# Kernel tuning notes

Measured on AMD Instinct MI355X. Metric: run time of the kernel, lower is better.

## Reference

```python
import jax, jax.numpy as jnp
import numpy as np

EPS = 1e-5


def conv1d(x, w, b):
    # x: (B, C_in, S), w: (C_out, C_in, K), 'same' padding = K//2
    pad = w.shape[-1] // 2
    y = jax.lax.conv_general_dilated(
        x, w, window_strides=(1,), padding=[(pad, pad)],
        dimension_numbers=("NCH", "OIH", "NCH"))
    return y + b[None, :, None]


def layer_norm(x, g, b):
    m = jnp.mean(x, axis=-1, keepdims=True)
    v = jnp.var(x, axis=-1, keepdims=True)
    return (x - m) * jax.lax.rsqrt(v + EPS) * g + b


def duration_predict(x, conv1_w, conv1_b, conv2_w, conv2_b,
                     ln1_g, ln1_b, ln2_g, ln2_b, lin_w, lin_b):
    # x: (B, S, C)
    out = conv1d(jnp.swapaxes(x, -2, -1), conv1_w, conv1_b)          # (B, F, S)
    out = jax.nn.relu(layer_norm(jnp.swapaxes(out, -2, -1), ln1_g, ln1_b))  # (B, S, F)
    out = conv1d(jnp.swapaxes(out, -2, -1), conv2_w, conv2_b)        # (B, F, S)
    out = jax.nn.relu(layer_norm(jnp.swapaxes(out, -2, -1), ln2_g, ln2_b))  # (B, S, F)
    out = jax.nn.relu(out @ lin_w.T + lin_b)                          # (B, S, 1)
    return jnp.squeeze(out, -1)                                       # (B, S)


def setup_inputs() -> dict:
    key = jax.random.key(0)
    ks = jax.random.split(key, 6)
    B, S, C = 16, 1024, 256
    F_, K = 256, 3
    inp = {
        "x": jax.random.normal(ks[0], (B, S, C), dtype=jnp.float32),
        "target": jax.random.uniform(ks[1], (B, S), dtype=jnp.float32),
        "conv1_w": jax.random.normal(ks[2], (F_, C, K), dtype=jnp.float32) * 0.02,
        "conv1_b": jnp.zeros((F_,), dtype=jnp.float32),
        "conv2_w": jax.random.normal(ks[3], (F_, F_, K), dtype=jnp.float32) * 0.02,
        "conv2_b": jnp.zeros((F_,), dtype=jnp.float32),
        "ln1_g": jnp.ones((F_,), dtype=jnp.float32),
        "ln1_b": jnp.zeros((F_,), dtype=jnp.float32),
        "ln2_g": jnp.ones((F_,), dtype=jnp.float32),
        "ln2_b": jnp.zeros((F_,), dtype=jnp.float32),
        "lin_w": jax.random.normal(ks[4], (1, F_), dtype=jnp.float32) * 0.02,
        "lin_b": jnp.zeros((1,), dtype=jnp.float32),
    }
    return inp


def reference(x, target, conv1_w, conv1_b, conv2_w, conv2_b,
              ln1_g, ln1_b, ln2_g, ln2_b, lin_w, lin_b):
    reg_len = duration_predict(x, conv1_w, conv1_b, conv2_w, conv2_b,
                               ln1_g, ln1_b, ln2_g, ln2_b, lin_w, lin_b)
    # Faithful to the original: max_len uses exp(target), the mask uses round(target).
    # max_len is data-dependent -> computed from concrete target (host-side, like the original).
    max_len = int(np.round(float(jnp.max(jnp.sum(jnp.exp(target), axis=-1)))))
    d = jnp.round(target)                 # (B, S) integer-valued durations (banker's rounding, like Python round)
    fin = jnp.cumsum(d, axis=-1)          # (B, S) end offsets
    start = fin - d                       # (B, S) start offsets
    t = jnp.arange(max_len, dtype=target.dtype)  # (T,)
    mask = ((t[None, None, :] >= start[..., None]) &
            (t[None, None, :] < fin[..., None])).astype(x.dtype)  # (B, S, T)
    # x.transpose @ mask -> (B, C, T) -> transpose -> (B, T, C)
    expanded = jnp.einsum("bsc,bst->btc", x, mask)
    return expanded, reg_len
```

## Files before the change

kernel.cpp:

```cpp
#include <hip/hip_runtime.h>
#include <hip/hip_bf16.h>

using frag_ab = __attribute__((ext_vector_type(8))) short;
using frag_cd = __attribute__((ext_vector_type(4))) float;

#define SLEN 1024
#define CDIM 256
#define KTOT 768

static __device__ __forceinline__ short f2bf(float f) {
    __hip_bfloat16 h = __float2bfloat16(f);
    return *reinterpret_cast<short*>(&h);
}

__global__ __launch_bounds__(1024) void scan_scatter_kernel(
    const float* __restrict__ target, int* __restrict__ src, int T)
{
    const int b = blockIdx.x;
    const int tid = threadIdx.x;

    for (int i = tid; i < T; i += 1024) src[b * T + i] = -1;

    const float tv = target[b * SLEN + tid];
    const int d = (int)rintf(tv);

    const int lane = tid & 63;
    const int wid = tid >> 6;
    int v = d;
#pragma unroll
    for (int off = 1; off < 64; off <<= 1) {
        int n = __shfl_up(v, off);
        if (lane >= off) v += n;
    }
    __shared__ int waveSum[16];
    if (lane == 63) waveSum[wid] = v;
    __syncthreads();
    if (tid < 16) {
        int wv = waveSum[tid];
#pragma unroll
        for (int off = 1; off < 16; off <<= 1) {
            int n = __shfl_up(wv, off);
            if (tid >= off) wv += n;
        }
        waveSum[tid] = wv;
    }
    __syncthreads();
    const int fin = v + (wid > 0 ? waveSum[wid - 1] : 0);
    const int start = fin - d;
    for (int t = start; t < fin; ++t)
        if (t >= 0 && t < T) src[b * T + t] = tid;
}

__global__ __launch_bounds__(256) void expand_kernel(
    const float* __restrict__ x, const int* __restrict__ src,
    float* __restrict__ out, int T)
{
    const int row = blockIdx.x * 4 + (threadIdx.x >> 6);
    const int lane = threadIdx.x & 63;
    const int nrows = 16 * T;
    if (row >= nrows) return;
    const int b = row / T;
    const int s = src[row];
    float4 val = make_float4(0.f, 0.f, 0.f, 0.f);
    if (s >= 0)
        val = *(const float4*)(x + ((size_t)(b * SLEN + s)) * CDIM + lane * 4);
    *(float4*)(out + (size_t)row * CDIM + lane * 4) = val;
}

__global__ __launch_bounds__(256) void repack_w2(
    const float* __restrict__ w1, __hip_bfloat16* __restrict__ bt1,
    const float* __restrict__ w2, __hip_bfloat16* __restrict__ bt2)
{
    const int f = blockIdx.y;
    const int which = blockIdx.x / 3;
    const int K = (blockIdx.x % 3) * 256 + threadIdx.x;
    const int k3 = K >> 8;
    const int c = K & 255;
    const float* w = which ? w2 : w1;
    __hip_bfloat16* bt = which ? bt2 : bt1;
    bt[f * KTOT + K] = __float2bfloat16(w[f * KTOT + c * 3 + k3]);
}

__global__ __launch_bounds__(512) void fused_conv(
    const float* __restrict__ x,
    const __hip_bfloat16* __restrict__ bt1,
    const __hip_bfloat16* __restrict__ bt2,
    const float* __restrict__ cb1, const float* __restrict__ g1, const float* __restrict__ be1,
    const float* __restrict__ cb2, const float* __restrict__ g2, const float* __restrict__ be2,
    const float* __restrict__ lw, const float* __restrict__ lb,
    float* __restrict__ reg_len)
{
    __shared__ __align__(16) unsigned char xt[82 * 512];
    __shared__ __align__(16) unsigned char yt[66 * 512];
    __shared__ float red[66][8][2];
    __shared__ float stats[66][2];

    const int tid = threadIdx.x;
    const int b = blockIdx.y;
    const int s0 = blockIdx.x * 64;

    const float* xin = x + (size_t)b * SLEN * CDIM;
    for (int ii = tid; ii < 68 * 32; ii += 512) {
        const int r = ii >> 5, cc = ii & 31;
        const int s = s0 - 2 + r;
        frag_ab v = {0, 0, 0, 0, 0, 0, 0, 0};
        if (s >= 0 && s < SLEN) {
            const float4* p = (const float4*)(xin + (size_t)s * CDIM + cc * 8);
            const float4 q0 = p[0], q1 = p[1];
            v[0] = f2bf(q0.x); v[1] = f2bf(q0.y); v[2] = f2bf(q0.z); v[3] = f2bf(q0.w);
            v[4] = f2bf(q1.x); v[5] = f2bf(q1.y); v[6] = f2bf(q1.z); v[7] = f2bf(q1.w);
        }
        *(frag_ab*)(xt + r * 512 + ((cc * 16) ^ ((r & 7) << 4))) = v;
    }
    __syncthreads();

    const int lane = tid & 63;
    const int wid = tid >> 6;
    const int l15 = lane & 15;
    const int lk = lane >> 4;
    const int fbase = wid * 32;

    frag_cd acc1[5][2];
#pragma unroll
    for (int mf = 0; mf < 5; ++mf) {
        acc1[mf][0] = {0.f, 0.f, 0.f, 0.f};
        acc1[mf][1] = {0.f, 0.f, 0.f, 0.f};
    }
    {
        const __hip_bfloat16* p0 = bt1 + (size_t)(fbase + l15) * KTOT + lk * 8;
        const __hip_bfloat16* p1 = p0 + 16 * KTOT;
#pragma unroll
        for (int kk = 0; kk < 24; ++kk) {
            const int k3 = kk >> 3;
            const int colbyte = (kk & 7) * 64 + lk * 16;
            const frag_ab bb0 = *(const frag_ab*)(p0 + kk * 32);
            const frag_ab bb1 = *(const frag_ab*)(p1 + kk * 32);
            frag_ab a[5];
#pragma unroll
            for (int mf = 0; mf < 5; ++mf) {
                const int r = mf * 16 + l15 + k3;
                a[mf] = *(const frag_ab*)(xt + r * 512 + (colbyte ^ ((r & 7) << 4)));
            }
#pragma unroll
            for (int mf = 0; mf < 5; ++mf) {
                acc1[mf][0] = __builtin_amdgcn_mfma_f32_16x16x32_bf16(a[mf], bb0, acc1[mf][0], 0, 0, 0);
                acc1[mf][1] = __builtin_amdgcn_mfma_f32_16x16x32_bf16(a[mf], bb1, acc1[mf][1], 0, 0, 0);
            }
        }
    }

    {
        const float bias0 = cb1[fbase + l15];
        const float bias1 = cb1[fbase + 16 + l15];
#pragma unroll
        for (int mf = 0; mf < 5; ++mf) {
#pragma unroll
            for (int j = 0; j < 4; ++j) {
                acc1[mf][0][j] += bias0;
                acc1[mf][1][j] += bias1;
                float p = acc1[mf][0][j] + acc1[mf][1][j];
                float q = acc1[mf][0][j] * acc1[mf][0][j] + acc1[mf][1][j] * acc1[mf][1][j];
#pragma unroll
                for (int m = 1; m < 16; m <<= 1) {
                    p += __shfl_xor(p, m);
                    q += __shfl_xor(q, m);
                }
                const bool valid = (mf < 4) || (lk == 0 && j < 2);
                if (l15 == 0 && valid) {
                    const int yr = mf * 16 + lk * 4 + j;
                    red[yr][wid][0] = p;
                    red[yr][wid][1] = q;
                }
            }
        }
    }
    __syncthreads();
    if (tid < 66) {
        float s = 0.f, q = 0.f;
#pragma unroll
        for (int wv = 0; wv < 8; ++wv) { s += red[tid][wv][0]; q += red[tid][wv][1]; }
        const float mean = s * (1.f / 256.f);
        const float var = q * (1.f / 256.f) - mean * mean;
        stats[tid][0] = mean;
        stats[tid][1] = rsqrtf(var + 1e-5f);
    }
    __syncthreads();

    {
        const float ga0 = g1[fbase + l15], ga1 = g1[fbase + 16 + l15];
        const float bb0 = be1[fbase + l15], bb1 = be1[fbase + 16 + l15];
        const int c0b = (fbase + l15) * 2;
        const int c1b = (fbase + 16 + l15) * 2;
#pragma unroll
        for (int mf = 0; mf < 5; ++mf) {
#pragma unroll
            for (int j = 0; j < 4; ++j) {
                const bool valid = (mf < 4) || (lk == 0 && j < 2);
                if (valid) {
                    const int yr = mf * 16 + lk * 4 + j;
                    const float mean = stats[yr][0], rs = stats[yr][1];
                    const float v0 = fmaxf((acc1[mf][0][j] - mean) * rs * ga0 + bb0, 0.f);
                    const float v1 = fmaxf((acc1[mf][1][j] - mean) * rs * ga1 + bb1, 0.f);
                    const int sw = (yr & 7) << 4;
                    *(short*)(yt + yr * 512 + (c0b ^ sw)) = f2bf(v0);
                    *(short*)(yt + yr * 512 + (c1b ^ sw)) = f2bf(v1);
                }
            }
        }
    }
    __syncthreads();
    if (blockIdx.x == 0 && tid < 32) {
        frag_ab z = {0, 0, 0, 0, 0, 0, 0, 0};
        *(frag_ab*)(yt + (tid * 16)) = z;
    }
    if (blockIdx.x == 15 && tid >= 64 && tid < 96) {
        frag_ab z = {0, 0, 0, 0, 0, 0, 0, 0};
        const int cc = tid - 64;
        *(frag_ab*)(yt + 65 * 512 + ((cc * 16) ^ ((65 & 7) << 4))) = z;
    }
    __syncthreads();

    frag_cd acc2[4][2];
#pragma unroll
    for (int mf = 0; mf < 4; ++mf) {
        acc2[mf][0] = {0.f, 0.f, 0.f, 0.f};
        acc2[mf][1] = {0.f, 0.f, 0.f, 0.f};
    }
    {
        const __hip_bfloat16* p0 = bt2 + (size_t)(fbase + l15) * KTOT + lk * 8;
        const __hip_bfloat16* p1 = p0 + 16 * KTOT;
#pragma unroll
        for (int kk = 0; kk < 24; ++kk) {
            const int k3 = kk >> 3;
            const int colbyte = (kk & 7) * 64 + lk * 16;
            const frag_ab bb0 = *(const frag_ab*)(p0 + kk * 32);
            const frag_ab bb1 = *(const frag_ab*)(p1 + kk * 32);
            frag_ab a[4];
#pragma unroll
            for (int mf = 0; mf < 4; ++mf) {
                const int r = mf * 16 + l15 + k3;
                a[mf] = *(const frag_ab*)(yt + r * 512 + (colbyte ^ ((r & 7) << 4)));
            }
#pragma unroll
            for (int mf = 0; mf < 4; ++mf) {
                acc2[mf][0] = __builtin_amdgcn_mfma_f32_16x16x32_bf16(a[mf], bb0, acc2[mf][0], 0, 0, 0);
                acc2[mf][1] = __builtin_amdgcn_mfma_f32_16x16x32_bf16(a[mf], bb1, acc2[mf][1], 0, 0, 0);
            }
        }
    }

    {
        const float bias0 = cb2[fbase + l15];
        const float bias1 = cb2[fbase + 16 + l15];
#pragma unroll
        for (int mf = 0; mf < 4; ++mf) {
#pragma unroll
            for (int j = 0; j < 4; ++j) {
                acc2[mf][0][j] += bias0;
                acc2[mf][1][j] += bias1;
                float p = acc2[mf][0][j] + acc2[mf][1][j];
                float q = acc2[mf][0][j] * acc2[mf][0][j] + acc2[mf][1][j] * acc2[mf][1][j];
#pragma unroll
                for (int m = 1; m < 16; m <<= 1) {
                    p += __shfl_xor(p, m);
                    q += __shfl_xor(q, m);
                }
                if (l15 == 0) {
                    const int row = mf * 16 + lk * 4 + j;
                    red[row][wid][0] = p;
                    red[row][wid][1] = q;
                }
            }
        }
    }
    __syncthreads();
    if (tid < 64) {
        float s = 0.f, q = 0.f;
#pragma unroll
        for (int wv = 0; wv < 8; ++wv) { s += red[tid][wv][0]; q += red[tid][wv][1]; }
        const float mean = s * (1.f / 256.f);
        const float var = q * (1.f / 256.f) - mean * mean;
        stats[tid][0] = mean;
        stats[tid][1] = rsqrtf(var + 1e-5f);
    }
    __syncthreads();

    {
        const float ga0 = g2[fbase + l15], ga1 = g2[fbase + 16 + l15];
        const float bb0 = be2[fbase + l15], bb1 = be2[fbase + 16 + l15];
        const float lw0 = lw[fbase + l15], lw1 = lw[fbase + 16 + l15];
#pragma unroll
        for (int mf = 0; mf < 4; ++mf) {
#pragma unroll
            for (int j = 0; j < 4; ++j) {
                const int row = mf * 16 + lk * 4 + j;
                const float mean = stats[row][0], rs = stats[row][1];
                const float v0 = fmaxf((acc2[mf][0][j] - mean) * rs * ga0 + bb0, 0.f);
                const float v1 = fmaxf((acc2[mf][1][j] - mean) * rs * ga1 + bb1, 0.f);
                float p = v0 * lw0 + v1 * lw1;
#pragma unroll
                for (int m = 1; m < 16; m <<= 1) p += __shfl_xor(p, m);
                if (l15 == 0) red[row][wid][0] = p;
            }
        }
    }
    __syncthreads();
    if (tid < 64) {
        float s = 0.f;
#pragma unroll
        for (int wv = 0; wv < 8; ++wv) s += red[tid][wv][0];
        reg_len[b * SLEN + s0 + tid] = fmaxf(s + lb[0], 0.f);
    }
}

extern "C" void kernel_launch(void* const* d_in, const int* in_sizes, int n_in,
                              void* d_out, int out_size, void* d_ws, size_t ws_size,
                              hipStream_t stream)
{
    const float* x       = (const float*)d_in[0];
    const float* target  = (const float*)d_in[1];
    const float* conv1_w = (const float*)d_in[2];
    const float* conv1_b = (const float*)d_in[3];
    const float* conv2_w = (const float*)d_in[4];
    const float* conv2_b = (const float*)d_in[5];
    const float* ln1_g   = (const float*)d_in[6];
    const float* ln1_b   = (const float*)d_in[7];
    const float* ln2_g   = (const float*)d_in[8];
    const float* ln2_b   = (const float*)d_in[9];
    const float* lin_w   = (const float*)d_in[10];
    const float* lin_b   = (const float*)d_in[11];

    const int B = 16, S = 1024, C = 256;
    const int T = (out_size - B * S) / (B * C);

    float* expanded = (float*)d_out;
    float* reg_len  = (float*)d_out + (size_t)B * T * C;

    unsigned char* ws = (unsigned char*)d_ws;
    __hip_bfloat16* bt1 = (__hip_bfloat16*)ws;
    __hip_bfloat16* bt2 = (__hip_bfloat16*)(ws + 393216);
    int* src = (int*)(ws + 2 * 393216);

    scan_scatter_kernel<<<B, 1024, 0, stream>>>(target, src, T);
    repack_w2<<<dim3(6, 256), 256, 0, stream>>>(conv1_w, bt1, conv2_w, bt2);

    fused_conv<<<dim3(16, 16), 512, 0, stream>>>(
        x, bt1, bt2, conv1_b, ln1_g, ln1_b, conv2_b, ln2_g, ln2_b,
        lin_w, lin_b, reg_len);

    expand_kernel<<<(B * T + 3) / 4, 256, 0, stream>>>(x, src, expanded, T);
}
```

Measured before the change: 57.07 us.

## Prefetch conv weight fragments in register ring and shrink LDS for two blocks per CU

Weight B-fragments for both conv GEMMs are now loaded from global memory into an 8-deep register ring ahead of use, and the conv2 weights are issued before the LayerNorm epilogue of conv1, to hide global load latency behind MFMA work. The x tile in shared memory shrinks from 82 to 68 rows, with the last A-fragment row index clamped to stay in bounds. Launch bounds now request 2 blocks per CU. The register prefetch buffers add substantial VGPR pressure, which together with the occupancy hint may cause spilling.

```diff
diff --git a/kernel.cpp b/kernel.cpp
--- a/kernel.cpp
+++ b/kernel.cpp
@@ -7,6 +7,7 @@
 #define SLEN 1024
 #define CDIM 256
 #define KTOT 768
+#define PD 8
 
 static __device__ __forceinline__ short f2bf(float f) {
     __hip_bfloat16 h = __float2bfloat16(f);
@@ -81,7 +82,7 @@
     bt[f * KTOT + K] = __float2bfloat16(w[f * KTOT + c * 3 + k3]);
 }
 
-__global__ __launch_bounds__(512) void fused_conv(
+__global__ __launch_bounds__(512, 2) void fused_conv(
     const float* __restrict__ x,
     const __hip_bfloat16* __restrict__ bt1,
     const __hip_bfloat16* __restrict__ bt2,
@@ -90,7 +91,7 @@
     const float* __restrict__ lw, const float* __restrict__ lb,
     float* __restrict__ reg_len)
 {
-    __shared__ __align__(16) unsigned char xt[82 * 512];
+    __shared__ __align__(16) unsigned char xt[68 * 512];
     __shared__ __align__(16) unsigned char yt[66 * 512];
     __shared__ float red[66][8][2];
     __shared__ float stats[66][2];
@@ -98,6 +99,21 @@
     const int tid = threadIdx.x;
     const int b = blockIdx.y;
     const int s0 = blockIdx.x * 64;
+
+    const int lane = tid & 63;
+    const int wid = tid >> 6;
+    const int l15 = lane & 15;
+    const int lk = lane >> 4;
+    const int fbase = wid * 32;
+
+    const __hip_bfloat16* p10 = bt1 + (size_t)(fbase + l15) * KTOT + lk * 8;
+    const __hip_bfloat16* p11 = p10 + 16 * KTOT;
+    frag_ab pb0[PD], pb1[PD];
+#pragma unroll
+    for (int i = 0; i < PD; ++i) {
+        pb0[i] = *(const frag_ab*)(p10 + i * 32);
+        pb1[i] = *(const frag_ab*)(p11 + i * 32);
+    }
 
     const float* xin = x + (size_t)b * SLEN * CDIM;
     for (int ii = tid; ii < 68 * 32; ii += 512) {
@@ -114,39 +130,43 @@
     }
     __syncthreads();
 
-    const int lane = tid & 63;
-    const int wid = tid >> 6;
-    const int l15 = lane & 15;
-    const int lk = lane >> 4;
-    const int fbase = wid * 32;
-
     frag_cd acc1[5][2];
 #pragma unroll
     for (int mf = 0; mf < 5; ++mf) {
         acc1[mf][0] = {0.f, 0.f, 0.f, 0.f};
         acc1[mf][1] = {0.f, 0.f, 0.f, 0.f};
     }
-    {
-        const __hip_bfloat16* p0 = bt1 + (size_t)(fbase + l15) * KTOT + lk * 8;
-        const __hip_bfloat16* p1 = p0 + 16 * KTOT;
-#pragma unroll
-        for (int kk = 0; kk < 24; ++kk) {
-            const int k3 = kk >> 3;
-            const int colbyte = (kk & 7) * 64 + lk * 16;
-            const frag_ab bb0 = *(const frag_ab*)(p0 + kk * 32);
-            const frag_ab bb1 = *(const frag_ab*)(p1 + kk * 32);
-            frag_ab a[5];
-#pragma unroll
-            for (int mf = 0; mf < 5; ++mf) {
-                const int r = mf * 16 + l15 + k3;
-                a[mf] = *(const frag_ab*)(xt + r * 512 + (colbyte ^ ((r & 7) << 4)));
-            }
-#pragma unroll
-            for (int mf = 0; mf < 5; ++mf) {
-                acc1[mf][0] = __builtin_amdgcn_mfma_f32_16x16x32_bf16(a[mf], bb0, acc1[mf][0], 0, 0, 0);
-                acc1[mf][1] = __builtin_amdgcn_mfma_f32_16x16x32_bf16(a[mf], bb1, acc1[mf][1], 0, 0, 0);
-            }
-        }
+#pragma unroll
+    for (int kk = 0; kk < 24; ++kk) {
+        const frag_ab bb0 = pb0[kk % PD];
+        const frag_ab bb1 = pb1[kk % PD];
+        if (kk + PD < 24) {
+            pb0[kk % PD] = *(const frag_ab*)(p10 + (kk + PD) * 32);
+            pb1[kk % PD] = *(const frag_ab*)(p11 + (kk + PD) * 32);
+        }
+        const int k3 = kk >> 3;
+        const int colbyte = (kk & 7) * 64 + lk * 16;
+        frag_ab a[5];
+#pragma unroll
+        for (int mf = 0; mf < 5; ++mf) {
+            int r = mf * 16 + l15 + k3;
+            if (mf == 4) r = (r > 67) ? 67 : r;
+            a[mf] = *(const frag_ab*)(xt + r * 512 + (colbyte ^ ((r & 7) << 4)));
+        }
+#pragma unroll
+        for (int mf = 0; mf < 5; ++mf) {
+            acc1[mf][0] = __builtin_amdgcn_mfma_f32_16x16x32_bf16(a[mf], bb0, acc1[mf][0], 0, 0, 0);
+            acc1[mf][1] = __builtin_amdgcn_mfma_f32_16x16x32_bf16(a[mf], bb1, acc1[mf][1], 0, 0, 0);
+        }
+    }
+
+    const __hip_bfloat16* p20 = bt2 + (size_t)(fbase + l15) * KTOT + lk * 8;
+    const __hip_bfloat16* p21 = p20 + 16 * KTOT;
+    frag_ab qb0[PD], qb1[PD];
+#pragma unroll
+    for (int i = 0; i < PD; ++i) {
+        qb0[i] = *(const frag_ab*)(p20 + i * 32);
+        qb1[i] = *(const frag_ab*)(p21 + i * 32);
     }
 
     {
@@ -226,26 +246,26 @@
         acc2[mf][0] = {0.f, 0.f, 0.f, 0.f};
         acc2[mf][1] = {0.f, 0.f, 0.f, 0.f};
     }
-    {
-        const __hip_bfloat16* p0 = bt2 + (size_t)(fbase + l15) * KTOT + lk * 8;
-        const __hip_bfloat16* p1 = p0 + 16 * KTOT;
-#pragma unroll
-        for (int kk = 0; kk < 24; ++kk) {
-            const int k3 = kk >> 3;
-            const int colbyte = (kk & 7) * 64 + lk * 16;
-            const frag_ab bb0 = *(const frag_ab*)(p0 + kk * 32);
-            const frag_ab bb1 = *(const frag_ab*)(p1 + kk * 32);
-            frag_ab a[4];
-#pragma unroll
-            for (int mf = 0; mf < 4; ++mf) {
-                const int r = mf * 16 + l15 + k3;
-                a[mf] = *(const frag_ab*)(yt + r * 512 + (colbyte ^ ((r & 7) << 4)));
-            }
-#pragma unroll
-            for (int mf = 0; mf < 4; ++mf) {
-                acc2[mf][0] = __builtin_amdgcn_mfma_f32_16x16x32_bf16(a[mf], bb0, acc2[mf][0], 0, 0, 0);
-                acc2[mf][1] = __builtin_amdgcn_mfma_f32_16x16x32_bf16(a[mf], bb1, acc2[mf][1], 0, 0, 0);
-            }
+#pragma unroll
+    for (int kk = 0; kk < 24; ++kk) {
+        const frag_ab bb0 = qb0[kk % PD];
+        const frag_ab bb1 = qb1[kk % PD];
+        if (kk + PD < 24) {
+            qb0[kk % PD] = *(const frag_ab*)(p20 + (kk + PD) * 32);
+            qb1[kk % PD] = *(const frag_ab*)(p21 + (kk + PD) * 32);
+        }
+        const int k3 = kk >> 3;
+        const int colbyte = (kk & 7) * 64 + lk * 16;
+        frag_ab a[4];
+#pragma unroll
+        for (int mf = 0; mf < 4; ++mf) {
+            const int r = mf * 16 + l15 + k3;
+            a[mf] = *(const frag_ab*)(yt + r * 512 + (colbyte ^ ((r & 7) << 4)));
+        }
+#pragma unroll
+        for (int mf = 0; mf < 4; ++mf) {
+            acc2[mf][0] = __builtin_amdgcn_mfma_f32_16x16x32_bf16(a[mf], bb0, acc2[mf][0], 0, 0, 0);
+            acc2[mf][1] = __builtin_amdgcn_mfma_f32_16x16x32_bf16(a[mf], bb1, acc2[mf][1], 0, 0, 0);
         }
     }
 
```

Measured after the change: 56.75 us. About the same (-0.6%).

## Retile fused conv waves into 2x4 row/column grid with register-prefetched weights

Applied to the files above, without the earlier changes.

Reassigns the 8 waves of the fused conv kernel from a 1x8 split over output channels (each wave covering all rows) to a 2x4 split over rows and 64-channel groups. This cuts the redundant LDS A-fragment reads per MFMA and halves the reduction partials per row. Weight fragments are prefetched into registers PD steps ahead, and the first batch is issued before the x tile load so global latency overlaps it. The change also shrinks LDS, folds the boundary-row zeroing into the LayerNorm store to drop a barrier, and requests 2 blocks per CU, at the cost of higher register pressure and uneven row work between the two wave groups.

```diff
diff --git a/kernel.cpp b/kernel.cpp
--- a/kernel.cpp
+++ b/kernel.cpp
@@ -7,6 +7,7 @@
 #define SLEN 1024
 #define CDIM 256
 #define KTOT 768
+#define PD 4
 
 static __device__ __forceinline__ short f2bf(float f) {
     __hip_bfloat16 h = __float2bfloat16(f);
@@ -81,7 +82,7 @@
     bt[f * KTOT + K] = __float2bfloat16(w[f * KTOT + c * 3 + k3]);
 }
 
-__global__ __launch_bounds__(512) void fused_conv(
+__global__ __launch_bounds__(512, 2) void fused_conv(
     const float* __restrict__ x,
     const __hip_bfloat16* __restrict__ bt1,
     const __hip_bfloat16* __restrict__ bt2,
@@ -90,14 +91,33 @@
     const float* __restrict__ lw, const float* __restrict__ lb,
     float* __restrict__ reg_len)
 {
-    __shared__ __align__(16) unsigned char xt[82 * 512];
+    __shared__ __align__(16) unsigned char xt[68 * 512];
     __shared__ __align__(16) unsigned char yt[66 * 512];
-    __shared__ float red[66][8][2];
+    __shared__ float red[66][9];
     __shared__ float stats[66][2];
 
     const int tid = threadIdx.x;
     const int b = blockIdx.y;
     const int s0 = blockIdx.x * 64;
+
+    const int lane = tid & 63;
+    const int wid = tid >> 6;
+    const int l15 = lane & 15;
+    const int lk = lane >> 4;
+    const int rg = wid >> 2;
+    const int cg = wid & 3;
+    const int fbase = cg * 64;
+
+    const __hip_bfloat16* p1[4];
+#pragma unroll
+    for (int n = 0; n < 4; ++n)
+        p1[n] = bt1 + (size_t)(fbase + n * 16 + l15) * KTOT + lk * 8;
+    frag_ab r1[4][PD];
+#pragma unroll
+    for (int i = 0; i < PD; ++i)
+#pragma unroll
+        for (int n = 0; n < 4; ++n)
+            r1[n][i] = *(const frag_ab*)(p1[n] + i * 32);
 
     const float* xin = x + (size_t)b * SLEN * CDIM;
     for (int ii = tid; ii < 68 * 32; ii += 512) {
@@ -114,62 +134,82 @@
     }
     __syncthreads();
 
-    const int lane = tid & 63;
-    const int wid = tid >> 6;
-    const int l15 = lane & 15;
-    const int lk = lane >> 4;
-    const int fbase = wid * 32;
-
-    frag_cd acc1[5][2];
-#pragma unroll
-    for (int mf = 0; mf < 5; ++mf) {
-        acc1[mf][0] = {0.f, 0.f, 0.f, 0.f};
-        acc1[mf][1] = {0.f, 0.f, 0.f, 0.f};
-    }
+    const int mb = rg * 3;
+    const int nf1 = 3 - rg;
+    frag_cd acc1[3][4];
+#pragma unroll
+    for (int mi = 0; mi < 3; ++mi)
+#pragma unroll
+        for (int n = 0; n < 4; ++n) acc1[mi][n] = {0.f, 0.f, 0.f, 0.f};
+
+#pragma unroll
+    for (int kk = 0; kk < 24; ++kk) {
+        frag_ab bb[4];
+#pragma unroll
+        for (int n = 0; n < 4; ++n) {
+            bb[n] = r1[n][kk % PD];
+            if (kk + PD < 24)
+                r1[n][kk % PD] = *(const frag_ab*)(p1[n] + (kk + PD) * 32);
+        }
+        const int k3 = kk >> 3;
+        const int colbyte = (kk & 7) * 64 + lk * 16;
+        frag_ab a[3];
+#pragma unroll
+        for (int mi = 0; mi < 3; ++mi) {
+            if (mi < nf1) {
+                int r = (mb + mi) * 16 + l15 + k3;
+                if (rg) r = (r > 67) ? 67 : r;
+                a[mi] = *(const frag_ab*)(xt + r * 512 + (colbyte ^ ((r & 7) << 4)));
+            }
+        }
+#pragma unroll
+        for (int mi = 0; mi < 3; ++mi) {
+            if (mi < nf1) {
+#pragma unroll
+                for (int n = 0; n < 4; ++n)
+                    acc1[mi][n] = __builtin_amdgcn_mfma_f32_16x16x32_bf16(a[mi], bb[n], acc1[mi][n], 0, 0, 0);
+            }
+        }
+    }
+
+    const __hip_bfloat16* p2[4];
+#pragma unroll
+    for (int n = 0; n < 4; ++n)
+        p2[n] = bt2 + (size_t)(fbase + n * 16 + l15) * KTOT + lk * 8;
+    frag_ab r2[4][PD];
+#pragma unroll
+    for (int i = 0; i < PD; ++i)
+#pragma unroll
+        for (int n = 0; n < 4; ++n)
+            r2[n][i] = *(const frag_ab*)(p2[n] + i * 32);
+
     {
-        const __hip_bfloat16* p0 = bt1 + (size_t)(fbase + l15) * KTOT + lk * 8;
-        const __hip_bfloat16* p1 = p0 + 16 * KTOT;
-#pragma unroll
-        for (int kk = 0; kk < 24; ++kk) {
-            const int k3 = kk >> 3;
-            const int colbyte = (kk & 7) * 64 + lk * 16;
-            const frag_ab bb0 = *(const frag_ab*)(p0 + kk * 32);
-            const frag_ab bb1 = *(const frag_ab*)(p1 + kk * 32);
-            frag_ab a[5];
-#pragma unroll
-            for (int mf = 0; mf < 5; ++mf) {
-                const int r = mf * 16 + l15 + k3;
-                a[mf] = *(const frag_ab*)(xt + r * 512 + (colbyte ^ ((r & 7) << 4)));
-            }
-#pragma unroll
-            for (int mf = 0; mf < 5; ++mf) {
-                acc1[mf][0] = __builtin_amdgcn_mfma_f32_16x16x32_bf16(a[mf], bb0, acc1[mf][0], 0, 0, 0);
-                acc1[mf][1] = __builtin_amdgcn_mfma_f32_16x16x32_bf16(a[mf], bb1, acc1[mf][1], 0, 0, 0);
-            }
-        }
-    }
-
-    {
-        const float bias0 = cb1[fbase + l15];
-        const float bias1 = cb1[fbase + 16 + l15];
-#pragma unroll
-        for (int mf = 0; mf < 5; ++mf) {
-#pragma unroll
-            for (int j = 0; j < 4; ++j) {
-                acc1[mf][0][j] += bias0;
-                acc1[mf][1][j] += bias1;
-                float p = acc1[mf][0][j] + acc1[mf][1][j];
-                float q = acc1[mf][0][j] * acc1[mf][0][j] + acc1[mf][1][j] * acc1[mf][1][j];
-#pragma unroll
-                for (int m = 1; m < 16; m <<= 1) {
-                    p += __shfl_xor(p, m);
-                    q += __shfl_xor(q, m);
-                }
-                const bool valid = (mf < 4) || (lk == 0 && j < 2);
-                if (l15 == 0 && valid) {
-                    const int yr = mf * 16 + lk * 4 + j;
-                    red[yr][wid][0] = p;
-                    red[yr][wid][1] = q;
+        float bv[4];
+#pragma unroll
+        for (int n = 0; n < 4; ++n) bv[n] = cb1[fbase + n * 16 + l15];
+#pragma unroll
+        for (int mi = 0; mi < 3; ++mi) {
+            if (mi < nf1) {
+#pragma unroll
+                for (int j = 0; j < 4; ++j) {
+                    float p = 0.f, q = 0.f;
+#pragma unroll
+                    for (int n = 0; n < 4; ++n) {
+                        acc1[mi][n][j] += bv[n];
+                        p += acc1[mi][n][j];
+                        q = fmaf(acc1[mi][n][j], acc1[mi][n][j], q);
+                    }
+#pragma unroll
+                    for (int m = 1; m < 16; m <<= 1) {
+                        p += __shfl_xor(p, m);
+                        q += __shfl_xor(q, m);
+                    }
+                    const bool valid = !(rg && mi == 1) || (lk == 0 && j < 2);
+                    if (l15 == 0 && valid) {
+                        const int yr = (mb + mi) * 16 + lk * 4 + j;
+                        red[yr][cg * 2] = p;
+                        red[yr][cg * 2 + 1] = q;
+                    }
                 }
             }
         }
@@ -178,7 +218,7 @@
     if (tid < 66) {
         float s = 0.f, q = 0.f;
 #pragma unroll
-        for (int wv = 0; wv < 8; ++wv) { s += red[tid][wv][0]; q += red[tid][wv][1]; }
+        for (int c = 0; c < 4; ++c) { s += red[tid][c * 2]; q += red[tid][c * 2 + 1]; }
         const float mean = s * (1.f / 256.f);
         const float var = q * (1.f / 256.f) - mean * mean;
         stats[tid][0] = mean;
@@ -187,88 +227,92 @@
     __syncthreads();
 
     {
-        const float ga0 = g1[fbase + l15], ga1 = g1[fbase + 16 + l15];
-        const float bb0 = be1[fbase + l15], bb1 = be1[fbase + 16 + l15];
-        const int c0b = (fbase + l15) * 2;
-        const int c1b = (fbase + 16 + l15) * 2;
-#pragma unroll
-        for (int mf = 0; mf < 5; ++mf) {
+        float ga[4], be[4];
+#pragma unroll
+        for (int n = 0; n < 4; ++n) {
+            ga[n] = g1[fbase + n * 16 + l15];
+            be[n] = be1[fbase + n * 16 + l15];
+        }
+#pragma unroll
+        for (int mi = 0; mi < 3; ++mi) {
+            if (mi < nf1) {
+#pragma unroll
+                for (int j = 0; j < 4; ++j) {
+                    const bool valid = !(rg && mi == 1) || (lk == 0 && j < 2);
+                    if (valid) {
+                        const int yr = (mb + mi) * 16 + lk * 4 + j;
+                        const float mean = stats[yr][0], rs = stats[yr][1];
+                        const bool zrow = (blockIdx.x == 0 && yr == 0) ||
+                                          (blockIdx.x == 15 && yr == 65);
+                        const int sw = (yr & 7) << 4;
+#pragma unroll
+                        for (int n = 0; n < 4; ++n) {
+                            float v = fmaxf((acc1[mi][n][j] - mean) * rs * ga[n] + be[n], 0.f);
+                            if (zrow) v = 0.f;
+                            *(short*)(yt + yr * 512 + (((fbase + n * 16 + l15) * 2) ^ sw)) = f2bf(v);
+                        }
+                    }
+                }
+            }
+        }
+    }
+    __syncthreads();
+
+    const int nb = rg * 2;
+    frag_cd acc2[2][4];
+#pragma unroll
+    for (int mi = 0; mi < 2; ++mi)
+#pragma unroll
+        for (int n = 0; n < 4; ++n) acc2[mi][n] = {0.f, 0.f, 0.f, 0.f};
+
+#pragma unroll
+    for (int kk = 0; kk < 24; ++kk) {
+        frag_ab bb[4];
+#pragma unroll
+        for (int n = 0; n < 4; ++n) {
+            bb[n] = r2[n][kk % PD];
+            if (kk + PD < 24)
+                r2[n][kk % PD] = *(const frag_ab*)(p2[n] + (kk + PD) * 32);
+        }
+        const int k3 = kk >> 3;
+        const int colbyte = (kk & 7) * 64 + lk * 16;
+        frag_ab a[2];
+#pragma unroll
+        for (int mi = 0; mi < 2; ++mi) {
+            const int r = (nb + mi) * 16 + l15 + k3;
+            a[mi] = *(const frag_ab*)(yt + r * 512 + (colbyte ^ ((r & 7) << 4)));
+        }
+#pragma unroll
+        for (int mi = 0; mi < 2; ++mi)
+#pragma unroll
+            for (int n = 0; n < 4; ++n)
+                acc2[mi][n] = __builtin_amdgcn_mfma_f32_16x16x32_bf16(a[mi], bb[n], acc2[mi][n], 0, 0, 0);
+    }
+
+    {
+        float bv[4];
+#pragma unroll
+        for (int n = 0; n < 4; ++n) bv[n] = cb2[fbase + n * 16 + l15];
+#pragma unroll
+        for (int mi = 0; mi < 2; ++mi) {
 #pragma unroll
             for (int j = 0; j < 4; ++j) {
-                const bool valid = (mf < 4) || (lk == 0 && j < 2);
-                if (valid) {
-                    const int yr = mf * 16 + lk * 4 + j;
-                    const float mean = stats[yr][0], rs = stats[yr][1];
-                    const float v0 = fmaxf((acc1[mf][0][j] - mean) * rs * ga0 + bb0, 0.f);
-                    const float v1 = fmaxf((acc1[mf][1][j] - mean) * rs * ga1 + bb1, 0.f);
-                    const int sw = (yr & 7) << 4;
-                    *(short*)(yt + yr * 512 + (c0b ^ sw)) = f2bf(v0);
-                    *(short*)(yt + yr * 512 + (c1b ^ sw)) = f2bf(v1);
-                }
-            }
-        }
-    }
-    __syncthreads();
-    if (blockIdx.x == 0 && tid < 32) {
-        frag_ab z = {0, 0, 0, 0, 0, 0, 0, 0};
-        *(frag_ab*)(yt + (tid * 16)) = z;
-    }
-    if (blockIdx.x == 15 && tid >= 64 && tid < 96) {
-        frag_ab z = {0, 0, 0, 0, 0, 0, 0, 0};
-        const int cc = tid - 64;
-        *(frag_ab*)(yt + 65 * 512 + ((cc * 16) ^ ((65 & 7) << 4))) = z;
-    }
-    __syncthreads();
-
-    frag_cd acc2[4][2];
-#pragma unroll
-    for (int mf = 0; mf < 4; ++mf) {
-        acc2[mf][0] = {0.f, 0.f, 0.f, 0.f};
-        acc2[mf][1] = {0.f, 0.f, 0.f, 0.f};
-    }
-    {
-        const __hip_bfloat16* p0 = bt2 + (size_t)(fbase + l15) * KTOT + lk * 8;
-        const __hip_bfloat16* p1 = p0 + 16 * KTOT;
-#pragma unroll
-        for (int kk = 0; kk < 24; ++kk) {
-            const int k3 = kk >> 3;
-            const int colbyte = (kk & 7) * 64 + lk * 16;
-            const frag_ab bb0 = *(const frag_ab*)(p0 + kk * 32);
-            const frag_ab bb1 = *(const frag_ab*)(p1 + kk * 32);
-            frag_ab a[4];
-#pragma unroll
-            for (int mf = 0; mf < 4; ++mf) {
-                const int r = mf * 16 + l15 + k3;
-                a[mf] = *(const frag_ab*)(yt + r * 512 + (colbyte ^ ((r & 7) << 4)));
-            }
-#pragma unroll
-            for (int mf = 0; mf < 4; ++mf) {
-                acc2[mf][0] = __builtin_amdgcn_mfma_f32_16x16x32_bf16(a[mf], bb0, acc2[mf][0], 0, 0, 0);
-                acc2[mf][1] = __builtin_amdgcn_mfma_f32_16x16x32_bf16(a[mf], bb1, acc2[mf][1], 0, 0, 0);
-            }
-        }
-    }
-
-    {
-        const float bias0 = cb2[fbase + l15];
-        const float bias1 = cb2[fbase + 16 + l15];
-#pragma unroll
-        for (int mf = 0; mf < 4; ++mf) {
-#pragma unroll
-            for (int j = 0; j < 4; ++j) {
-                acc2[mf][0][j] += bias0;
-                acc2[mf][1][j] += bias1;
-                float p = acc2[mf][0][j] + acc2[mf][1][j];
-                float q = acc2[mf][0][j] * acc2[mf][0][j] + acc2[mf][1][j] * acc2[mf][1][j];
+                float p = 0.f, q = 0.f;
+#pragma unroll
+                for (int n = 0; n < 4; ++n) {
+                    acc2[mi][n][j] += bv[n];
+                    p += acc2[mi][n][j];
+                    q = fmaf(acc2[mi][n][j], acc2[mi][n][j], q);
+                }
 #pragma unroll
                 for (int m = 1; m < 16; m <<= 1) {
                     p += __shfl_xor(p, m);
                     q += __shfl_xor(q, m);
                 }
                 if (l15 == 0) {
-                    const int row = mf * 16 + lk * 4 + j;
-                    red[row][wid][0] = p;
-                    red[row][wid][1] = q;
+                    const int row = (nb + mi) * 16 + lk * 4 + j;
+                    red[row][cg * 2] = p;
+                    red[row][cg * 2 + 1] = q;
                 }
             }
         }
@@ -277,7 +321,7 @@
     if (tid < 64) {
         float s = 0.f, q = 0.f;
 #pragma unroll
-        for (int wv = 0; wv < 8; ++wv) { s += red[tid][wv][0]; q += red[tid][wv][1]; }
+        for (int c = 0; c < 4; ++c) { s += red[tid][c * 2]; q += red[tid][c * 2 + 1]; }
         const float mean = s * (1.f / 256.f);
         const float var = q * (1.f / 256.f) - mean * mean;
         stats[tid][0] = mean;
@@ -286,21 +330,28 @@
     __syncthreads();
 
     {
-        const float ga0 = g2[fbase + l15], ga1 = g2[fbase + 16 + l15];
-        const float bb0 = be2[fbase + l15], bb1 = be2[fbase + 16 + l15];
-        const float lw0 = lw[fbase + l15], lw1 = lw[fbase + 16 + l15];
-#pragma unroll
-        for (int mf = 0; mf < 4; ++mf) {
+        float ga[4], be[4], lv[4];
+#pragma unroll
+        for (int n = 0; n < 4; ++n) {
+            ga[n] = g2[fbase + n * 16 + l15];
+            be[n] = be2[fbase + n * 16 + l15];
+            lv[n] = lw[fbase + n * 16 + l15];
+        }
+#pragma unroll
+        for (int mi = 0; mi < 2; ++mi) {
 #pragma unroll
             for (int j = 0; j < 4; ++j) {
-                const int row = mf * 16 + lk * 4 + j;
+                const int row = (nb + mi) * 16 + lk * 4 + j;
                 const float mean = stats[row][0], rs = stats[row][1];
-                const float v0 = fmaxf((acc2[mf][0][j] - mean) * rs * ga0 + bb0, 0.f);
-                const float v1 = fmaxf((acc2[mf][1][j] - mean) * rs * ga1 + bb1, 0.f);
-                float p = v0 * lw0 + v1 * lw1;
+                float p = 0.f;
+#pragma unroll
+                for (int n = 0; n < 4; ++n) {
+                    const float v = fmaxf((acc2[mi][n][j] - mean) * rs * ga[n] + be[n], 0.f);
+                    p = fmaf(v, lv[n], p);
+                }
 #pragma unroll
                 for (int m = 1; m < 16; m <<= 1) p += __shfl_xor(p, m);
-                if (l15 == 0) red[row][wid][0] = p;
+                if (l15 == 0) red[row][cg * 2] = p;
             }
         }
     }
@@ -308,7 +359,7 @@
     if (tid < 64) {
         float s = 0.f;
 #pragma unroll
-        for (int wv = 0; wv < 8; ++wv) s += red[tid][wv][0];
+        for (int c = 0; c < 4; ++c) s += red[tid][c * 2];
         reg_len[b * SLEN + s0 + tid] = fmaxf(s + lb[0], 0.f);
     }
 }
```

Measured after the change: 72.13 us. +26.4%, slower.
